# Optimization experiments

Hardware: AMD Instinct MI355X
Metric: run time of the kernel (lower is better)

Reference implementation:

```python
import jax, jax.numpy as jnp
import numpy as np

DECAY = 0.99
EPS = 1e-05


def setup_inputs() -> dict:
    key = jax.random.key(0)
    k1, k2, k3 = jax.random.split(key, 3)
    inputs = jax.random.normal(k1, (16, 32, 32, 128), dtype=jnp.float32)
    cluster_mean = jax.random.normal(k2, (128, 10000), dtype=jnp.float32)
    cluster_sum = jax.random.normal(k3, (128, 10000), dtype=jnp.float32)
    cluster_size = jnp.zeros((10000,), dtype=jnp.float32)
    return {"inputs": inputs, "cluster_mean": cluster_mean,
            "cluster_sum": cluster_sum, "cluster_size": cluster_size}


def reference(inputs, cluster_mean, cluster_sum, cluster_size):
    embed_dim, n_embed = cluster_mean.shape
    samples = inputs.reshape(-1, embed_dim)                      # [N, E]

    # squared-euclidean distance to each codebook entry: [N, K]
    dist = (jnp.sum(samples ** 2, axis=1, keepdims=True)
            - 2.0 * samples @ cluster_mean
            + jnp.sum(cluster_mean ** 2, axis=0, keepdims=True))
    cluster_index = jnp.argmin(dist, axis=1)                     # [N] int

    # EMA statistics (segment-sum instead of materializing [N, K] one-hot)
    counts = jax.ops.segment_sum(jnp.ones_like(cluster_index, dtype=samples.dtype),
                                 cluster_index, num_segments=n_embed)      # [K]
    sums = jax.ops.segment_sum(samples, cluster_index, num_segments=n_embed).T  # [E, K]

    new_cluster_size = cluster_size * DECAY + counts * (1.0 - DECAY)
    new_cluster_sum = cluster_sum * DECAY + sums * (1.0 - DECAY)

    n_sample = jnp.sum(new_cluster_size)
    smoothed = (new_cluster_size + EPS) * n_sample / (n_sample + n_embed * EPS)
    new_cluster_mean = new_cluster_sum / smoothed                # [E, K]

    idx_grid = cluster_index.reshape(inputs.shape[:-1])          # [B, H, W]
    quantize = new_cluster_mean.T[idx_grid]                      # [B, H, W, E]

    e_loss = jnp.mean((inputs - jax.lax.stop_gradient(quantize)) ** 2)
    outputs = inputs + jax.lax.stop_gradient(quantize - inputs)  # straight-through
    return outputs, 0.25 * e_loss, new_cluster_mean, new_cluster_size, new_cluster_sum
```

## Files before the change

kernel.cpp:

```cpp
#include <hip/hip_runtime.h>

#define NS 16384
#define ED 128
#define KC 10000
#define KP 10240
#define EKTOT (ED*KC)

#define O_OUT  0
#define O_LOSS (NS*ED)
#define O_MEAN (O_LOSS+1)
#define O_SIZE (O_MEAN+EKTOT)
#define O_SUM  (O_SIZE+KC)

#define WB_BEST  0u
#define WB_CNORM 131072u
#define WB_IDX   172032u
#define WB_CNT   237568u
#define WB_NS    278528u
#define WB_XH    294912u
#define WB_XL    4489216u
#define WB_MH    8683520u
#define WB_ML    11304960u

typedef _Float16 f16;
typedef _Float16 f16x8 __attribute__((ext_vector_type(8)));
typedef _Float16 f16x4 __attribute__((ext_vector_type(4)));
typedef float f32x4 __attribute__((ext_vector_type(4)));

constexpr float DECAY = 0.99f;
constexpr float OMD   = 0.01f;
constexpr float EPSV  = 1e-5f;

__global__ void k_prep(const float* __restrict__ X, const float* __restrict__ M,
                       const float* __restrict__ CZ,
                       f16* __restrict__ Xh, f16* __restrict__ Xl,
                       f16* __restrict__ Mh, f16* __restrict__ Ml,
                       float* __restrict__ cnorm, float* __restrict__ cnt,
                       unsigned long long* __restrict__ best,
                       float* __restrict__ out, float* __restrict__ ns_cz) {
    const int b = blockIdx.x, t = threadIdx.x;
    if (b < 2048) {
        int i = (b * 256 + t) * 4;
        float4 v = *(const float4*)(X + i);
        f16x4 h, l;
        h[0] = (f16)v.x; l[0] = (f16)(v.x - (float)h[0]);
        h[1] = (f16)v.y; l[1] = (f16)(v.y - (float)h[1]);
        h[2] = (f16)v.z; l[2] = (f16)(v.z - (float)h[2]);
        h[3] = (f16)v.w; l[3] = (f16)(v.w - (float)h[3]);
        *(f16x4*)(Xh + i) = h;
        *(f16x4*)(Xl + i) = l;
        if (t < 160) {
            int f4 = b * 160 + t;
            if (f4 * 4 < EKTOT) *(float4*)(out + f4 * 4) = make_float4(0.f, 0.f, 0.f, 0.f);
        }
    } else if (b < 2088) {
        int k = (b - 2048) * 256 + t;
        float s = __builtin_inff();
        if (k < KC) {
            s = 0.f;
            #pragma unroll
            for (int c = 0; c < 16; ++c) {
                f16x8 h, l;
                #pragma unroll
                for (int j = 0; j < 8; ++j) {
                    float m = M[(size_t)(c * 8 + j) * KC + k];
                    s = fmaf(m, m, s);
                    h[j] = (f16)m;
                    l[j] = (f16)(m - (float)h[j]);
                }
                *(f16x8*)(Mh + (size_t)k * ED + c * 8) = h;
                *(f16x8*)(Ml + (size_t)k * ED + c * 8) = l;
            }
        } else {
            f16x8 z = {0, 0, 0, 0, 0, 0, 0, 0};
            #pragma unroll
            for (int c = 0; c < 16; ++c) {
                *(f16x8*)(Mh + (size_t)k * ED + c * 8) = z;
                *(f16x8*)(Ml + (size_t)k * ED + c * 8) = z;
            }
        }
        cnorm[k] = s;
        cnt[k] = 0.f;
        for (int i = k; i < NS; i += 40 * 256) best[i] = ~0ull;
    } else {
        __shared__ float red[256];
        float s = 0.f;
        for (int i = t; i < KC; i += 256) s += CZ[i];
        red[t] = s;
        __syncthreads();
        for (int st = 128; st > 0; st >>= 1) {
            if (t < st) red[t] += red[t + st];
            __syncthreads();
        }
        if (t == 0) { *ns_cz = red[0]; out[O_LOSS] = 0.f; }
    }
}

__launch_bounds__(256, 2)
__global__ void k_assign(const f16* __restrict__ Xh, const f16* __restrict__ Xl,
                         const f16* __restrict__ Mh, const f16* __restrict__ Ml,
                         const float* __restrict__ cnorm,
                         unsigned long long* __restrict__ best) {
    __shared__ f16 Bs[128 * 64];

    const int c0 = blockIdx.x * 128;
    const int n0 = blockIdx.y * 128;

    const int t = threadIdx.x, w = t >> 6, l = t & 63;
    const int wr = w >> 1, wc = w & 1;
    const int lg = l >> 4, li = l & 15;

    f32x4 acc[4][4];
    #pragma unroll
    for (int i = 0; i < 4; ++i)
        #pragma unroll
        for (int j = 0; j < 4; ++j) acc[i][j] = (f32x4)0.f;

    const f16* Ap[6] = {Xh, Xh, Xl, Xh, Xh, Xl};
    const f16* Bp[6] = {Mh, Ml, Mh, Mh, Ml, Mh};

    f16x8 a[4][2];

    for (int st = 0; st < 6; ++st) {
        const int hh = st < 3 ? 0 : 1;
        const bool loadA = (st != 1) && (st != 4);
        const f16* A = Ap[st];
        const f16* B = Bp[st];

        if (loadA) {
            #pragma unroll
            for (int i = 0; i < 4; ++i)
                #pragma unroll
                for (int ks = 0; ks < 2; ++ks)
                    a[i][ks] = *(const f16x8*)(A + (size_t)(n0 + wr * 64 + i * 16 + li) * ED
                                               + hh * 64 + ks * 32 + lg * 8);
        }

        __syncthreads();
        #pragma unroll
        for (int it = 0; it < 4; ++it) {
            int f = it * 256 + t;
            int row = f >> 3, seg = f & 7;
            int segS = seg ^ (row & 7);
            const f16* gb = B + (size_t)(c0 + row) * ED + hh * 64 + segS * 8;
            f16* lb = Bs + (it * 256 + w * 64) * 8;
            __builtin_amdgcn_global_load_lds(
                (const __attribute__((address_space(1))) unsigned int*)gb,
                (__attribute__((address_space(3))) unsigned int*)lb, 16, 0, 0);
        }
        __syncthreads();

        #pragma unroll
        for (int ks = 0; ks < 2; ++ks) {
            f16x8 bfr[4];
            #pragma unroll
            for (int j = 0; j < 4; ++j) {
                int r = wc * 64 + j * 16 + li;
                bfr[j] = *(const f16x8*)(Bs + r * 64 + ((ks * 32 + lg * 8) ^ ((r & 7) << 3)));
            }
            #pragma unroll
            for (int i = 0; i < 4; ++i)
                #pragma unroll
                for (int j = 0; j < 4; ++j)
                    acc[i][j] = __builtin_amdgcn_mfma_f32_16x16x32_f16(a[i][ks], bfr[j], acc[i][j], 0, 0, 0);
        }
    }

    float cn[4];
    #pragma unroll
    for (int j = 0; j < 4; ++j) cn[j] = cnorm[c0 + wc * 64 + j * 16 + li];

    #pragma unroll
    for (int i = 0; i < 4; ++i) {
        #pragma unroll
        for (int r = 0; r < 4; ++r) {
            float bv = __builtin_inff(); int bc = 0;
            #pragma unroll
            for (int j = 0; j < 4; ++j) {
                int c = c0 + wc * 64 + j * 16 + li;
                float d = fmaf(-2.f, acc[i][j][r], cn[j]);
                if (d < bv) { bv = d; bc = c; }
            }
            #pragma unroll
            for (int off = 1; off < 16; off <<= 1) {
                float v2 = __shfl_xor(bv, off);
                int   c2 = __shfl_xor(bc, off);
                if (v2 < bv || (v2 == bv && c2 < bc)) { bv = v2; bc = c2; }
            }
            if (li == 0) {
                unsigned u = __float_as_uint(bv);
                u = (u & 0x80000000u) ? ~u : (u | 0x80000000u);
                unsigned long long key = ((unsigned long long)u << 32) | (unsigned)bc;
                atomicMin(best + (n0 + wr * 64 + i * 16 + lg * 4 + r), key);
            }
        }
    }
}

__global__ void k_scatter(const float* __restrict__ X,
                          const unsigned long long* __restrict__ best,
                          int* __restrict__ idx,
                          float* __restrict__ sumT, float* __restrict__ cnt) {
    int tt = blockIdx.x * 256 + threadIdx.x;
    int n = tt >> 7, e = tt & 127;
    int k = (int)(unsigned)(best[n] & 0xFFFFFFFFull);
    if (e == 0) { idx[n] = k; atomicAdd(cnt + k, 1.0f); }
    atomicAdd(sumT + (size_t)k * ED + e, X[tt] * OMD);
}

__global__ void k_mean(const float* __restrict__ csum, const float* __restrict__ csize,
                       const float* __restrict__ cnt, const float* __restrict__ ns_cz,
                       float* __restrict__ out, float* __restrict__ meanT) {
    __shared__ float lds[64 * 129];
    const int k0 = blockIdx.x * 64;
    const int t = threadIdx.x;
    const float* sumT = out;

    #pragma unroll
    for (int r = 0; r < 32; ++r) {
        int f = r * 256 + t;
        int kl = f >> 7, e = f & 127;
        float v = (k0 + kl < KC) ? sumT[(size_t)(k0 + kl) * ED + e] : 0.f;
        lds[kl * 129 + e] = v;
    }
    __syncthreads();

    const int kl2 = t & 63, ww = t >> 6;
    const int k = k0 + kl2;
    if (k < KC) {
        float nsz = fmaf(csize[k], DECAY, cnt[k] * OMD);
        if (ww == 0) out[O_SIZE + k] = nsz;
        float ns  = fmaf(*ns_cz, DECAY, OMD * (float)NS);
        float sm  = (nsz + EPSV) * ns / (ns + (float)KC * EPSV);
        float inv = 1.f / sm;
        #pragma unroll
        for (int r2 = 0; r2 < 32; ++r2) {
            int e2 = r2 * 4 + ww;
            float s   = lds[kl2 * 129 + e2];
            float ncs = fmaf(csum[(size_t)e2 * KC + k], DECAY, s);
            out[O_SUM  + (size_t)e2 * KC + k] = ncs;
            float mean = ncs * inv;
            out[O_MEAN + (size_t)e2 * KC + k] = mean;
            lds[kl2 * 129 + e2] = mean;
        }
    }
    __syncthreads();

    #pragma unroll
    for (int r = 0; r < 32; ++r) {
        int f = r * 256 + t;
        int kl = f >> 7, e = f & 127;
        if (k0 + kl < KC) meanT[(size_t)(k0 + kl) * ED + e] = lds[kl * 129 + e];
    }
}

__global__ void k_gather(const float* __restrict__ X, const int* __restrict__ idx,
                         const float* __restrict__ meanT, float* __restrict__ out) {
    __shared__ float red[256];
    int tt = blockIdx.x * 256 + threadIdx.x;
    int n = tt >> 7, e = tt & 127;
    int k = idx[n];
    float q = meanT[(size_t)k * ED + e];
    float x = X[tt];
    out[O_OUT + tt] = x + (q - x);
    float d = x - q;
    red[threadIdx.x] = d * d;
    __syncthreads();
    for (int s = 128; s > 0; s >>= 1) {
        if (threadIdx.x < s) red[threadIdx.x] += red[threadIdx.x + s];
        __syncthreads();
    }
    if (threadIdx.x == 0)
        atomicAdd(out + O_LOSS, red[0] * (0.25f / (float)(NS * ED)));
}

extern "C" void kernel_launch(void* const* d_in, const int* in_sizes, int n_in,
                              void* d_out, int out_size, void* d_ws, size_t ws_size,
                              hipStream_t stream) {
    const float* X  = (const float*)d_in[0];
    const float* M  = (const float*)d_in[1];
    const float* CS = (const float*)d_in[2];
    const float* CZ = (const float*)d_in[3];
    float* out = (float*)d_out;

    char* wsb = (char*)d_ws;
    unsigned long long* best = (unsigned long long*)(wsb + WB_BEST);
    float* cnorm = (float*)(wsb + WB_CNORM);
    int*   idx   = (int*)(wsb + WB_IDX);
    float* cnt   = (float*)(wsb + WB_CNT);
    float* ns_cz = (float*)(wsb + WB_NS);
    f16* Xh = (f16*)(wsb + WB_XH);
    f16* Xl = (f16*)(wsb + WB_XL);
    f16* Mh = (f16*)(wsb + WB_MH);
    f16* Ml = (f16*)(wsb + WB_ML);
    float* sumT  = out;
    float* meanT = (float*)(wsb + WB_XH);

    hipLaunchKernelGGL(k_prep,   dim3(2089),               dim3(256), 0, stream,
                       X, M, CZ, Xh, Xl, Mh, Ml, cnorm, cnt, best, out, ns_cz);
    hipLaunchKernelGGL(k_assign, dim3(KP / 128, NS / 128), dim3(256), 0, stream,
                       Xh, Xl, Mh, Ml, cnorm, best);
    hipLaunchKernelGGL(k_scatter,dim3(NS * ED / 256),      dim3(256), 0, stream,
                       X, best, idx, sumT, cnt);
    hipLaunchKernelGGL(k_mean,   dim3((KC + 63) / 64),     dim3(256), 0, stream,
                       CS, CZ, cnt, ns_cz, out, meanT);
    hipLaunchKernelGGL(k_gather, dim3(NS * ED / 256),      dim3(256), 0, stream,
                       X, idx, meanT, out);
}
```

Measured before the change: 450.4 us.

## Stage A and B hi/lo tiles together in LDS, cut to two sync rounds

The assign GEMM used to run six stages, each loading one B tile into LDS with a barrier pair and loading A fragments straight from global memory. Now each K-half loads Xh, Xl, Mh and Ml tiles into four swizzled LDS buffers at once, then runs the three hi/lo MFMA passes from LDS. This cuts barrier rounds from six to two, turns uncoalesced direct A loads into async LDS copies, and issues more loads in flight together. In exchange LDS use rises from 16KB to 64KB per block, which may limit occupancy (launch bounds ask for 2 blocks per CU), and more A registers are live.

```diff
diff --git a/kernel.cpp b/kernel.cpp
--- a/kernel.cpp
+++ b/kernel.cpp
@@ -101,7 +101,10 @@
                          const f16* __restrict__ Mh, const f16* __restrict__ Ml,
                          const float* __restrict__ cnorm,
                          unsigned long long* __restrict__ best) {
-    __shared__ f16 Bs[128 * 64];
+    __shared__ f16 AsH[128 * 64];
+    __shared__ f16 AsL[128 * 64];
+    __shared__ f16 BsH[128 * 64];
+    __shared__ f16 BsL[128 * 64];
 
     const int c0 = blockIdx.x * 128;
     const int n0 = blockIdx.y * 128;
@@ -116,53 +119,65 @@
         #pragma unroll
         for (int j = 0; j < 4; ++j) acc[i][j] = (f32x4)0.f;
 
-    const f16* Ap[6] = {Xh, Xh, Xl, Xh, Xh, Xl};
-    const f16* Bp[6] = {Mh, Ml, Mh, Mh, Ml, Mh};
-
-    f16x8 a[4][2];
-
-    for (int st = 0; st < 6; ++st) {
-        const int hh = st < 3 ? 0 : 1;
-        const bool loadA = (st != 1) && (st != 4);
-        const f16* A = Ap[st];
-        const f16* B = Bp[st];
-
-        if (loadA) {
-            #pragma unroll
-            for (int i = 0; i < 4; ++i)
-                #pragma unroll
-                for (int ks = 0; ks < 2; ++ks)
-                    a[i][ks] = *(const f16x8*)(A + (size_t)(n0 + wr * 64 + i * 16 + li) * ED
-                                               + hh * 64 + ks * 32 + lg * 8);
-        }
-
+    for (int hh = 0; hh < 2; ++hh) {
         __syncthreads();
         #pragma unroll
         for (int it = 0; it < 4; ++it) {
             int f = it * 256 + t;
             int row = f >> 3, seg = f & 7;
             int segS = seg ^ (row & 7);
-            const f16* gb = B + (size_t)(c0 + row) * ED + hh * 64 + segS * 8;
-            f16* lb = Bs + (it * 256 + w * 64) * 8;
+            size_t goffA = (size_t)(n0 + row) * ED + hh * 64 + segS * 8;
+            size_t goffB = (size_t)(c0 + row) * ED + hh * 64 + segS * 8;
+            int loff = (it * 256 + w * 64) * 8;
             __builtin_amdgcn_global_load_lds(
-                (const __attribute__((address_space(1))) unsigned int*)gb,
-                (__attribute__((address_space(3))) unsigned int*)lb, 16, 0, 0);
+                (const __attribute__((address_space(1))) unsigned int*)(Xh + goffA),
+                (__attribute__((address_space(3))) unsigned int*)(AsH + loff), 16, 0, 0);
+            __builtin_amdgcn_global_load_lds(
+                (const __attribute__((address_space(1))) unsigned int*)(Xl + goffA),
+                (__attribute__((address_space(3))) unsigned int*)(AsL + loff), 16, 0, 0);
+            __builtin_amdgcn_global_load_lds(
+                (const __attribute__((address_space(1))) unsigned int*)(Mh + goffB),
+                (__attribute__((address_space(3))) unsigned int*)(BsH + loff), 16, 0, 0);
+            __builtin_amdgcn_global_load_lds(
+                (const __attribute__((address_space(1))) unsigned int*)(Ml + goffB),
+                (__attribute__((address_space(3))) unsigned int*)(BsL + loff), 16, 0, 0);
         }
         __syncthreads();
 
-        #pragma unroll
-        for (int ks = 0; ks < 2; ++ks) {
-            f16x8 bfr[4];
-            #pragma unroll
-            for (int j = 0; j < 4; ++j) {
-                int r = wc * 64 + j * 16 + li;
-                bfr[j] = *(const f16x8*)(Bs + r * 64 + ((ks * 32 + lg * 8) ^ ((r & 7) << 3)));
-            }
-            #pragma unroll
-            for (int i = 0; i < 4; ++i)
+        f16x8 ah[4][2], al[4][2];
+        #pragma unroll
+        for (int i = 0; i < 4; ++i) {
+            int r = wr * 64 + i * 16 + li;
+            #pragma unroll
+            for (int ks = 0; ks < 2; ++ks) {
+                int off = r * 64 + ((ks * 32 + lg * 8) ^ ((r & 7) << 3));
+                ah[i][ks] = *(const f16x8*)(AsH + off);
+                al[i][ks] = *(const f16x8*)(AsL + off);
+            }
+        }
+
+        #pragma unroll
+        for (int p = 0; p < 3; ++p) {
+            const f16* bs = (p == 1) ? BsL : BsH;
+            #pragma unroll
+            for (int ks = 0; ks < 2; ++ks) {
+                f16x8 bfr[4];
                 #pragma unroll
-                for (int j = 0; j < 4; ++j)
-                    acc[i][j] = __builtin_amdgcn_mfma_f32_16x16x32_f16(a[i][ks], bfr[j], acc[i][j], 0, 0, 0);
+                for (int j = 0; j < 4; ++j) {
+                    int r = wc * 64 + j * 16 + li;
+                    bfr[j] = *(const f16x8*)(bs + r * 64 + ((ks * 32 + lg * 8) ^ ((r & 7) << 3)));
+                }
+                #pragma unroll
+                for (int i = 0; i < 4; ++i) {
+                    #pragma unroll
+                    for (int j = 0; j < 4; ++j) {
+                        if (p == 2)
+                            acc[i][j] = __builtin_amdgcn_mfma_f32_16x16x32_f16(al[i][ks], bfr[j], acc[i][j], 0, 0, 0);
+                        else
+                            acc[i][j] = __builtin_amdgcn_mfma_f32_16x16x32_f16(ah[i][ks], bfr[j], acc[i][j], 0, 0, 0);
+                    }
+                }
+            }
         }
     }
 
```

After: 498.8 us. +10.7%, slower.

## Pre-swizzle X fp16 splits into fragment layout and split k_mean across embed chunks

Applied to the files above, without the earlier changes.

k_prep now stages X through LDS and writes the fp16 hi/lo split in a fragment-ordered layout. This lets k_assign load its A operands as contiguous coalesced 16-byte chunks instead of row-strided loads. k_assign's launch bounds rise from 2 to 3 waves per SIMD, which lowers the register budget and risks spills. k_mean is split into four embed-dim chunks per 64-cluster block, giving a smaller LDS footprint and four times as many blocks for better parallelism.

```diff
diff --git a/kernel.cpp b/kernel.cpp
--- a/kernel.cpp
+++ b/kernel.cpp
@@ -33,28 +33,46 @@
 
 __global__ void k_prep(const float* __restrict__ X, const float* __restrict__ M,
                        const float* __restrict__ CZ,
-                       f16* __restrict__ Xh, f16* __restrict__ Xl,
+                       f16* __restrict__ XhF, f16* __restrict__ XlF,
                        f16* __restrict__ Mh, f16* __restrict__ Ml,
                        float* __restrict__ cnorm, float* __restrict__ cnt,
                        unsigned long long* __restrict__ best,
                        float* __restrict__ out, float* __restrict__ ns_cz) {
     const int b = blockIdx.x, t = threadIdx.x;
-    if (b < 2048) {
-        int i = (b * 256 + t) * 4;
-        float4 v = *(const float4*)(X + i);
-        f16x4 h, l;
-        h[0] = (f16)v.x; l[0] = (f16)(v.x - (float)h[0]);
-        h[1] = (f16)v.y; l[1] = (f16)(v.y - (float)h[1]);
-        h[2] = (f16)v.z; l[2] = (f16)(v.z - (float)h[2]);
-        h[3] = (f16)v.w; l[3] = (f16)(v.w - (float)h[3]);
-        *(f16x4*)(Xh + i) = h;
-        *(f16x4*)(Xl + i) = l;
-        if (t < 160) {
-            int f4 = b * 160 + t;
-            if (f4 * 4 < EKTOT) *(float4*)(out + f4 * 4) = make_float4(0.f, 0.f, 0.f, 0.f);
-        }
-    } else if (b < 2088) {
-        int k = (b - 2048) * 256 + t;
+    if (b < 512) {
+        __shared__ float xl[32 * 132];
+        const int n0 = b * 32;
+        #pragma unroll
+        for (int it = 0; it < 4; ++it) {
+            int f = it * 256 + t;
+            int nl = f >> 5, e4 = (f & 31) << 2;
+            float4 v = *(const float4*)(X + (size_t)(n0 + nl) * ED + e4);
+            xl[nl * 132 + e4 + 0] = v.x;
+            xl[nl * 132 + e4 + 1] = v.y;
+            xl[nl * 132 + e4 + 2] = v.z;
+            xl[nl * 132 + e4 + 3] = v.w;
+        }
+        __syncthreads();
+        #pragma unroll
+        for (int ot = 0; ot < 2; ++ot) {
+            int idx = ot * 256 + t;
+            int li = idx & 15, o = (idx >> 4) & 15, nbl = idx >> 8;
+            const float* src = &xl[(nbl * 16 + li) * 132 + o * 8];
+            f16x8 h, l;
+            #pragma unroll
+            for (int j = 0; j < 8; ++j) {
+                float v = src[j];
+                h[j] = (f16)v;
+                l[j] = (f16)(v - (float)h[j]);
+            }
+            size_t dst = (size_t)(b * 2 + nbl) * 2048 + o * 128 + li * 8;
+            *(f16x8*)(XhF + dst) = h;
+            *(f16x8*)(XlF + dst) = l;
+        }
+        for (int i4 = b * 256 + t; i4 < EKTOT / 4; i4 += 512 * 256)
+            *(float4*)(out + i4 * 4) = make_float4(0.f, 0.f, 0.f, 0.f);
+    } else if (b < 552) {
+        int k = (b - 512) * 256 + t;
         float s = __builtin_inff();
         if (k < KC) {
             s = 0.f;
@@ -96,8 +114,8 @@
     }
 }
 
-__launch_bounds__(256, 2)
-__global__ void k_assign(const f16* __restrict__ Xh, const f16* __restrict__ Xl,
+__launch_bounds__(256, 3)
+__global__ void k_assign(const f16* __restrict__ XhF, const f16* __restrict__ XlF,
                          const f16* __restrict__ Mh, const f16* __restrict__ Ml,
                          const float* __restrict__ cnorm,
                          unsigned long long* __restrict__ best) {
@@ -116,7 +134,7 @@
         #pragma unroll
         for (int j = 0; j < 4; ++j) acc[i][j] = (f32x4)0.f;
 
-    const f16* Ap[6] = {Xh, Xh, Xl, Xh, Xh, Xl};
+    const f16* Ap[6] = {XhF, XhF, XlF, XhF, XhF, XlF};
     const f16* Bp[6] = {Mh, Ml, Mh, Mh, Ml, Mh};
 
     f16x8 a[4][2];
@@ -132,8 +150,9 @@
             for (int i = 0; i < 4; ++i)
                 #pragma unroll
                 for (int ks = 0; ks < 2; ++ks)
-                    a[i][ks] = *(const f16x8*)(A + (size_t)(n0 + wr * 64 + i * 16 + li) * ED
-                                               + hh * 64 + ks * 32 + lg * 8);
+                    a[i][ks] = *(const f16x8*)(A + (size_t)n0 * 128
+                                               + (wr * 4 + i) * 2048
+                                               + (hh * 8 + ks * 4 + lg) * 128 + li * 8);
         }
 
         __syncthreads();
@@ -211,17 +230,18 @@
 __global__ void k_mean(const float* __restrict__ csum, const float* __restrict__ csize,
                        const float* __restrict__ cnt, const float* __restrict__ ns_cz,
                        float* __restrict__ out, float* __restrict__ meanT) {
-    __shared__ float lds[64 * 129];
-    const int k0 = blockIdx.x * 64;
+    __shared__ float lds[64 * 33];
+    const int kb = blockIdx.x >> 2, ch = blockIdx.x & 3;
+    const int k0 = kb * 64, e0 = ch * 32;
     const int t = threadIdx.x;
     const float* sumT = out;
 
     #pragma unroll
-    for (int r = 0; r < 32; ++r) {
+    for (int r = 0; r < 8; ++r) {
         int f = r * 256 + t;
-        int kl = f >> 7, e = f & 127;
-        float v = (k0 + kl < KC) ? sumT[(size_t)(k0 + kl) * ED + e] : 0.f;
-        lds[kl * 129 + e] = v;
+        int kl = f >> 5, el = f & 31;
+        float v = (k0 + kl < KC) ? sumT[(size_t)(k0 + kl) * ED + e0 + el] : 0.f;
+        lds[kl * 33 + el] = v;
     }
     __syncthreads();
 
@@ -229,28 +249,28 @@
     const int k = k0 + kl2;
     if (k < KC) {
         float nsz = fmaf(csize[k], DECAY, cnt[k] * OMD);
-        if (ww == 0) out[O_SIZE + k] = nsz;
+        if (ch == 0 && ww == 0) out[O_SIZE + k] = nsz;
         float ns  = fmaf(*ns_cz, DECAY, OMD * (float)NS);
         float sm  = (nsz + EPSV) * ns / (ns + (float)KC * EPSV);
         float inv = 1.f / sm;
         #pragma unroll
-        for (int r2 = 0; r2 < 32; ++r2) {
-            int e2 = r2 * 4 + ww;
-            float s   = lds[kl2 * 129 + e2];
+        for (int r2 = 0; r2 < 8; ++r2) {
+            int e2 = e0 + r2 * 4 + ww;
+            float s   = lds[kl2 * 33 + (e2 - e0)];
             float ncs = fmaf(csum[(size_t)e2 * KC + k], DECAY, s);
             out[O_SUM  + (size_t)e2 * KC + k] = ncs;
             float mean = ncs * inv;
             out[O_MEAN + (size_t)e2 * KC + k] = mean;
-            lds[kl2 * 129 + e2] = mean;
+            lds[kl2 * 33 + (e2 - e0)] = mean;
         }
     }
     __syncthreads();
 
     #pragma unroll
-    for (int r = 0; r < 32; ++r) {
+    for (int r = 0; r < 8; ++r) {
         int f = r * 256 + t;
-        int kl = f >> 7, e = f & 127;
-        if (k0 + kl < KC) meanT[(size_t)(k0 + kl) * ED + e] = lds[kl * 129 + e];
+        int kl = f >> 5, el = f & 31;
+        if (k0 + kl < KC) meanT[(size_t)(k0 + kl) * ED + e0 + el] = lds[kl * 33 + el];
     }
 }
 
@@ -289,20 +309,20 @@
     int*   idx   = (int*)(wsb + WB_IDX);
     float* cnt   = (float*)(wsb + WB_CNT);
     float* ns_cz = (float*)(wsb + WB_NS);
-    f16* Xh = (f16*)(wsb + WB_XH);
-    f16* Xl = (f16*)(wsb + WB_XL);
-    f16* Mh = (f16*)(wsb + WB_MH);
-    f16* Ml = (f16*)(wsb + WB_ML);
+    f16* XhF = (f16*)(wsb + WB_XH);
+    f16* XlF = (f16*)(wsb + WB_XL);
+    f16* Mh  = (f16*)(wsb + WB_MH);
+    f16* Ml  = (f16*)(wsb + WB_ML);
     float* sumT  = out;
     float* meanT = (float*)(wsb + WB_XH);
 
-    hipLaunchKernelGGL(k_prep,   dim3(2089),               dim3(256), 0, stream,
-                       X, M, CZ, Xh, Xl, Mh, Ml, cnorm, cnt, best, out, ns_cz);
+    hipLaunchKernelGGL(k_prep,   dim3(553),                dim3(256), 0, stream,
+                       X, M, CZ, XhF, XlF, Mh, Ml, cnorm, cnt, best, out, ns_cz);
     hipLaunchKernelGGL(k_assign, dim3(KP / 128, NS / 128), dim3(256), 0, stream,
-                       Xh, Xl, Mh, Ml, cnorm, best);
+                       XhF, XlF, Mh, Ml, cnorm, best);
     hipLaunchKernelGGL(k_scatter,dim3(NS * ED / 256),      dim3(256), 0, stream,
                        X, best, idx, sumT, cnt);
-    hipLaunchKernelGGL(k_mean,   dim3((KC + 63) / 64),     dim3(256), 0, stream,
+    hipLaunchKernelGGL(k_mean,   dim3(((KC + 63) / 64) * 4), dim3(256), 0, stream,
                        CS, CZ, cnt, ns_cz, out, meanT);
     hipLaunchKernelGGL(k_gather, dim3(NS * ED / 256),      dim3(256), 0, stream,
                        X, idx, meanT, out);
```

Measured after the change: 373.3 us. 1.21x faster.
